# Performance work log

Hardware: AMD Instinct MI355X
Metric: run time of the kernel (lower is better)

The kernel has to match this reference:

```python
import jax, jax.numpy as jnp
import numpy as np

B = 4
T, Hh, Ww = 16, 32, 32
C = 256
HEADS = 8
WIN = 4
SHIFT = 2
MLP = 1024


def _rel_pos_index(w):
    coords = np.stack(np.meshgrid(np.arange(w), np.arange(w), np.arange(w), indexing='ij')).reshape(3, -1)
    rc = (coords[:, :, None] - coords[:, None, :]).transpose(1, 2, 0)
    rc[:, :, 0] += w - 1
    rc[:, :, 1] += w - 1
    rc[:, :, 2] += w - 1
    rc[:, :, 0] *= (2 * w - 1) * (2 * w - 1)
    rc[:, :, 1] *= 2 * w - 1
    return rc.sum(-1).astype(np.int32)  # (w^3, w^3)


def _attn_mask(t, h, w, win, shift):
    m = np.zeros((t, h, w))
    sl = (slice(0, -win), slice(-win, -shift), slice(-shift, None))
    cnt = 0
    for a in sl:
        for b in sl:
            for c in sl:
                m[a, b, c] = cnt
                cnt += 1
    m = m.reshape(t // win, win, h // win, win, w // win, win).transpose(0, 2, 4, 1, 3, 5).reshape(-1, win ** 3)
    am = m[:, None, :] - m[:, :, None]  # (nW, N, N)
    return np.where(am != 0, -100.0, 0.0).astype(np.float32)


def setup_inputs() -> dict:
    key = jax.random.key(0)
    ks = jax.random.split(key, 12)
    s_in = 1.0 / np.sqrt(C)
    s_mlp = 1.0 / np.sqrt(MLP)
    return {
        'x': jax.random.normal(ks[0], (B, T * Hh * Ww, C), jnp.float32),
        'norm1_g': jnp.ones((C,), jnp.float32),
        'norm1_b': jnp.zeros((C,), jnp.float32),
        'qkv_w': jax.random.normal(ks[1], (C, 3 * C), jnp.float32) * s_in,
        'qkv_b': jax.random.normal(ks[2], (3 * C,), jnp.float32) * 0.02,
        'proj_w': jax.random.normal(ks[3], (C, C), jnp.float32) * s_in,
        'proj_b': jax.random.normal(ks[4], (C,), jnp.float32) * 0.02,
        'rel_bias_table': jax.random.normal(ks[5], ((2 * WIN - 1) ** 3, HEADS), jnp.float32) * 0.02,
        'norm2_g': jnp.ones((C,), jnp.float32),
        'norm2_b': jnp.zeros((C,), jnp.float32),
        'mlp_w1': jax.random.normal(ks[6], (C, MLP), jnp.float32) * s_in,
        'mlp_b1': jax.random.normal(ks[7], (MLP,), jnp.float32) * 0.02,
        'mlp_w2': jax.random.normal(ks[8], (MLP, C), jnp.float32) * s_mlp,
        'mlp_b2': jax.random.normal(ks[9], (C,), jnp.float32) * 0.02,
        'rel_index': jnp.asarray(_rel_pos_index(WIN)),
        'attn_mask': jnp.asarray(_attn_mask(T, Hh, Ww, WIN, SHIFT)),
    }


def _ln(x, g, b, eps):
    mu = x.mean(-1, keepdims=True)
    var = ((x - mu) ** 2).mean(-1, keepdims=True)
    return (x - mu) * jax.lax.rsqrt(var + eps) * g + b


def reference(x, norm1_g, norm1_b, qkv_w, qkv_b, proj_w, proj_b, rel_bias_table,
              norm2_g, norm2_b, mlp_w1, mlp_b1, mlp_w2, mlp_b2, rel_index, attn_mask):
    w = WIN
    N = w ** 3
    hd = C // HEADS
    scale = hd ** -0.5

    h = _ln(x, norm1_g, norm1_b, 1e-5).reshape(B, T, Hh, Ww, C)
    h = jnp.roll(h, shift=(-SHIFT, -SHIFT, -SHIFT), axis=(1, 2, 3))
    # window partition -> (B*nW, N, C)
    h = h.reshape(B, T // w, w, Hh // w, w, Ww // w, w, C)
    h = h.transpose(0, 1, 3, 5, 2, 4, 6, 7).reshape(-1, N, C)

    qkv = (h @ qkv_w + qkv_b).reshape(-1, N, 3, HEADS, hd)
    qkv = qkv.transpose(2, 0, 3, 1, 4)  # (3, BW, heads, N, hd)
    q, k, v = qkv[0] * scale, qkv[1], qkv[2]
    attn = jnp.einsum('bhid,bhjd->bhij', q, k)

    bias = rel_bias_table[rel_index.reshape(-1)].reshape(N, N, HEADS).transpose(2, 0, 1)
    attn = attn + bias[None]

    nW = attn_mask.shape[0]
    attn = attn.reshape(-1, nW, HEADS, N, N) + attn_mask[None, :, None]
    attn = jax.nn.softmax(attn.reshape(-1, HEADS, N, N), axis=-1)

    o = jnp.einsum('bhij,bhjd->bhid', attn, v).transpose(0, 2, 1, 3).reshape(-1, N, C)
    o = o @ proj_w + proj_b
    # window reverse
    o = o.reshape(B, T // w, Hh // w, Ww // w, w, w, w, C)
    o = o.transpose(0, 1, 4, 2, 5, 3, 6, 7).reshape(B, T, Hh, Ww, C)
    o = jnp.roll(o, shift=(SHIFT, SHIFT, SHIFT), axis=(1, 2, 3)).reshape(B, T * Hh * Ww, C)

    x = x + o
    y = _ln(x, norm2_g, norm2_b, 1e-6)
    y = jax.nn.gelu(y @ mlp_w1 + mlp_b1, approximate=False) @ mlp_w2 + mlp_b2
    return x + y
```

## Files before the change

kernel.cpp:

```cpp
#include <hip/hip_runtime.h>
#include <cstdint>
#include <cstddef>

typedef float  f32x4_t  __attribute__((ext_vector_type(4)));
typedef __bf16 bf16x8_t __attribute__((ext_vector_type(8)));
typedef __bf16 bf16x4_t __attribute__((ext_vector_type(4)));

#define NTOK   65536
#define CCH    256
#define NWINT  1024

__device__ __forceinline__ float wred_sum(float v) {
#pragma unroll
  for (int off = 32; off > 0; off >>= 1) v += __shfl_xor(v, off, 64);
  return v;
}

__device__ __forceinline__ void gload16(void* lds, const void* g) {
  __builtin_amdgcn_global_load_lds(
      (const __attribute__((address_space(1))) uint32_t*)g,
      (__attribute__((address_space(3))) uint32_t*)lds, 16, 0, 0);
}

__device__ __forceinline__ int win_to_orig(int token) {
  int gid = token >> 6, n = token & 63;
  int bb = gid >> 8, rem = gid & 255;
  int t = (((rem >> 6) << 2) + (n >> 4) + 2) & 15;
  int h = ((((rem >> 3) & 7) << 2) + ((n >> 2) & 3) + 2) & 31;
  int w = (((rem & 7) << 2) + (n & 3) + 2) & 31;
  return ((bb * 16 + t) * 32 + h) * 32 + w;
}

__device__ __forceinline__ float gelu_f(float v) {
  float u = v * (0.7978845608028654f + 0.03567740814f * v * v);
  float t = 1.0f - 2.0f / (__expf(2.0f * u) + 1.0f);
  return 0.5f * v * (1.0f + t);
}

#define MFMA16(ACC, W, Af)                                              \
  _Pragma("unroll") for (int nn = 0; nn < 4; ++nn)                      \
      _Pragma("unroll") for (int mm = 0; mm < 4; ++mm)                  \
          ACC[nn][mm] = __builtin_amdgcn_mfma_f32_16x16x32_bf16(        \
              W[nn], Af[mm], ACC[nn][mm], 0, 0, 0);

__global__ __launch_bounds__(256) void prep_weights(
    const float* __restrict__ qkv_w, const float* __restrict__ proj_w,
    const float* __restrict__ mlp_w1, const float* __restrict__ mlp_w2,
    __bf16* __restrict__ wt_qkv, __bf16* __restrict__ wt_proj,
    __bf16* __restrict__ wt_mlp1, __bf16* __restrict__ wt_mlp2) {
  int i = blockIdx.x * 256 + threadIdx.x;
  if (i < 196608) {
    int k = i / 768, n = i % 768;
    wt_qkv[n * 256 + k] = (__bf16)qkv_w[i];
  } else if (i < 262144) {
    int j = i - 196608;
    int k = j >> 8, n = j & 255;
    wt_proj[n * 256 + k] = (__bf16)proj_w[j];
  } else if (i < 524288) {
    int j = i - 262144;
    int k = j >> 10, n = j & 1023;
    wt_mlp1[n * 256 + k] = (__bf16)mlp_w1[j];
  } else {
    int j = i - 524288;
    int k = j >> 8, n = j & 255;
    wt_mlp2[n * 1024 + k] = (__bf16)mlp_w2[j];
  }
}

__global__ __launch_bounds__(256) void cm_prep(
    const float* __restrict__ table, const int* __restrict__ ridx,
    const float* __restrict__ mask, __bf16* __restrict__ cm) {
  int tid = blockIdx.x * 256 + threadIdx.x;
  int l = tid & 63;
  int t16 = (tid >> 6) & 15;
  int h = (tid >> 10) & 7;
  int w = tid >> 13;
  int it = t16 & 3, jt = t16 >> 2;
  int i = it * 16 + (l & 15);
  int jb = jt * 16 + ((l >> 4) << 2);
  const float* mrow = mask + (size_t)w * 4096 + i * 64;
  const int* rrow = ridx + i * 64;
  bf16x4_t o;
#pragma unroll
  for (int r = 0; r < 4; ++r) {
    int j = jb + r;
    o[r] = (__bf16)(table[rrow[j] * 8 + h] + mrow[j]);
  }
  *(bf16x4_t*)(cm + (size_t)tid * 4) = o;
}

__global__ __launch_bounds__(256) void ln_kernel(
    const float* __restrict__ xin, const float* __restrict__ g,
    const float* __restrict__ b, __bf16* __restrict__ out, float eps) {
  int token = blockIdx.x * 4 + (threadIdx.x >> 6);
  int lane = threadIdx.x & 63;
  size_t src = (size_t)win_to_orig(token);
  f32x4_t v = ((const f32x4_t*)(xin + src * CCH))[lane];
  float mu = wred_sum(v[0] + v[1] + v[2] + v[3]) * (1.0f / 256.0f);
  float d0 = v[0] - mu, d1 = v[1] - mu, d2 = v[2] - mu, d3 = v[3] - mu;
  float var = wred_sum(d0 * d0 + d1 * d1 + d2 * d2 + d3 * d3) * (1.0f / 256.0f);
  float rs = rsqrtf(var + eps);
  f32x4_t gg = ((const f32x4_t*)g)[lane];
  f32x4_t bb = ((const f32x4_t*)b)[lane];
  bf16x4_t o;
  o[0] = (__bf16)(d0 * rs * gg[0] + bb[0]);
  o[1] = (__bf16)(d1 * rs * gg[1] + bb[1]);
  o[2] = (__bf16)(d2 * rs * gg[2] + bb[2]);
  o[3] = (__bf16)(d3 * rs * gg[3] + bb[3]);
  *(bf16x4_t*)(out + (size_t)token * CCH + lane * 4) = o;
}


__device__ __forceinline__ void stage_A64(__bf16* yA, const __bf16* A,
                                          int bm, int tid) {
#pragma unroll
  for (int rnd = 0; rnd < 8; ++rnd) {
    int slot = rnd * 256 + tid;
    int row = slot >> 5;
    int cb = ((slot & 31) << 4) ^ ((row & 7) << 4);
    gload16((char*)yA + slot * 16,
            (const char*)(A + (size_t)(bm + row) * 256) + cb);
  }
  asm volatile("s_waitcnt vmcnt(0)" ::: "memory");
  __syncthreads();
}

__global__ __launch_bounds__(256, 3) void gemm_qkv(
    const __bf16* __restrict__ A, const __bf16* __restrict__ Bt,
    const float* __restrict__ bias, __bf16* __restrict__ outp) {
  __shared__ __bf16 yA[64 * 256];
  const int wv = threadIdx.x >> 6;
  const int ln = threadIdx.x & 63;
  const int i15 = ln & 15, g = ln >> 4;
  const int sw = (i15 & 7) << 4;

  int nwg = gridDim.x;
  int wgid = ((int)blockIdx.x & 7) * (nwg >> 3) + ((int)blockIdx.x >> 3);
  int bx = wgid % 3, by = wgid / 3;
  const int bm = by * 64, bn = bx * 256;

  stage_A64(yA, A, bm, (int)threadIdx.x);

  const __bf16* wP[4];
#pragma unroll
  for (int q = 0; q < 4; ++q)
    wP[q] = Bt + (size_t)(bn + wv * 64 + q * 16 + i15) * 256 + g * 8;

  f32x4_t acc[4][4];
#pragma unroll
  for (int nn = 0; nn < 4; ++nn)
#pragma unroll
    for (int mm = 0; mm < 4; ++mm) acc[nn][mm] = (f32x4_t){0.f, 0.f, 0.f, 0.f};

#pragma unroll
  for (int kt = 0; kt < 4; ++kt)
#pragma unroll
    for (int kh = 0; kh < 2; ++kh) {
      bf16x8_t wf[4], af[4];
#pragma unroll
      for (int nn = 0; nn < 4; ++nn)
        wf[nn] = *(const bf16x8_t*)(wP[nn] + kt * 64 + kh * 32);
#pragma unroll
      for (int mm = 0; mm < 4; ++mm)
        af[mm] = *(const bf16x8_t*)((const char*)yA + (mm * 16 + i15) * 512 +
                                    ((kt * 128 + kh * 64 + g * 16) ^ sw));
      MFMA16(acc, wf, af);
    }

#pragma unroll
  for (int nn = 0; nn < 4; ++nn) {
    int colg = bn + wv * 64 + nn * 16 + g * 4;
    f32x4_t bv = *(const f32x4_t*)(bias + colg);
#pragma unroll
    for (int mm = 0; mm < 4; ++mm) {
      int rowg = bm + mm * 16 + i15;
      bf16x4_t o;
#pragma unroll
      for (int r = 0; r < 4; ++r) o[r] = (__bf16)(acc[nn][mm][r] + bv[r]);
      *(bf16x4_t*)(outp + (size_t)rowg * 768 + colg) = o;
    }
  }
}

__global__ __launch_bounds__(256, 3) void proj_ln(
    const __bf16* __restrict__ A, const __bf16* __restrict__ Bt,
    const float* __restrict__ bias, const float* __restrict__ res,
    const float* __restrict__ g2, const float* __restrict__ b2,
    __bf16* __restrict__ x2b, __bf16* __restrict__ yb) {
  __shared__ __bf16 yA[64 * 256];
  __shared__ float2 stf[256];
  const int wv = threadIdx.x >> 6;
  const int ln = threadIdx.x & 63;
  const int i15 = ln & 15, g = ln >> 4;
  const int sw = (i15 & 7) << 4;

  int nwg = gridDim.x;
  int wgid = ((int)blockIdx.x & 7) * (nwg >> 3) + ((int)blockIdx.x >> 3);
  const int bm = wgid * 64;

  stage_A64(yA, A, bm, (int)threadIdx.x);

  const __bf16* wP[4];
#pragma unroll
  for (int q = 0; q < 4; ++q)
    wP[q] = Bt + (size_t)(wv * 64 + q * 16 + i15) * 256 + g * 8;

  f32x4_t acc[4][4];
#pragma unroll
  for (int nn = 0; nn < 4; ++nn)
#pragma unroll
    for (int mm = 0; mm < 4; ++mm) acc[nn][mm] = (f32x4_t){0.f, 0.f, 0.f, 0.f};

#pragma unroll
  for (int kt = 0; kt < 4; ++kt)
#pragma unroll
    for (int kh = 0; kh < 2; ++kh) {
      bf16x8_t wf[4], af[4];
#pragma unroll
      for (int nn = 0; nn < 4; ++nn)
        wf[nn] = *(const bf16x8_t*)(wP[nn] + kt * 64 + kh * 32);
#pragma unroll
      for (int mm = 0; mm < 4; ++mm)
        af[mm] = *(const bf16x8_t*)((const char*)yA + (mm * 16 + i15) * 512 +
                                    ((kt * 128 + kh * 64 + g * 16) ^ sw));
      MFMA16(acc, wf, af);
    }

  size_t dst[4];
#pragma unroll
  for (int mm = 0; mm < 4; ++mm)
    dst[mm] = (size_t)win_to_orig(bm + mm * 16 + i15) * CCH;
#pragma unroll
  for (int nn = 0; nn < 4; ++nn) {
    int colg = wv * 64 + nn * 16 + g * 4;
    f32x4_t bv = *(const f32x4_t*)(bias + colg);
#pragma unroll
    for (int mm = 0; mm < 4; ++mm) {
      f32x4_t rv = *(const f32x4_t*)(res + dst[mm] + colg);
#pragma unroll
      for (int r = 0; r < 4; ++r) acc[nn][mm][r] += bv[r] + rv[r];
    }
  }

#pragma unroll
  for (int mm = 0; mm < 4; ++mm) {
    float s1 = 0.f, s2 = 0.f;
#pragma unroll
    for (int nn = 0; nn < 4; ++nn)
#pragma unroll
      for (int r = 0; r < 4; ++r) {
        float v = acc[nn][mm][r];
        s1 += v;
        s2 += v * v;
      }
    s1 += __shfl_xor(s1, 16, 64);
    s1 += __shfl_xor(s1, 32, 64);
    s2 += __shfl_xor(s2, 16, 64);
    s2 += __shfl_xor(s2, 32, 64);
    if (g == 0) stf[(mm * 16 + i15) * 4 + wv] = make_float2(s1, s2);
  }
  __syncthreads();
  float mu[4], rs[4];
#pragma unroll
  for (int mm = 0; mm < 4; ++mm) {
    int row = mm * 16 + i15;
    float S1 = 0.f, S2 = 0.f;
#pragma unroll
    for (int w = 0; w < 4; ++w) {
      float2 p = stf[row * 4 + w];
      S1 += p.x;
      S2 += p.y;
    }
    mu[mm] = S1 * (1.0f / 256.0f);
    rs[mm] = rsqrtf(S2 * (1.0f / 256.0f) - mu[mm] * mu[mm] + 1e-6f);
  }

#pragma unroll
  for (int nn = 0; nn < 4; ++nn) {
    int colg = wv * 64 + nn * 16 + g * 4;
    f32x4_t gv = *(const f32x4_t*)(g2 + colg);
    f32x4_t bv = *(const f32x4_t*)(b2 + colg);
#pragma unroll
    for (int mm = 0; mm < 4; ++mm) {
      f32x4_t v = acc[nn][mm];
      bf16x4_t xo, yo;
#pragma unroll
      for (int r = 0; r < 4; ++r) {
        xo[r] = (__bf16)v[r];
        yo[r] = (__bf16)((v[r] - mu[mm]) * rs[mm] * gv[r] + bv[r]);
      }
      *(bf16x4_t*)(x2b + dst[mm] + colg) = xo;
      *(bf16x4_t*)(yb + dst[mm] + colg) = yo;
    }
  }
}

__global__ __launch_bounds__(256, 2) void mlp_fused(
    const __bf16* __restrict__ yb, const __bf16* __restrict__ w1t,
    const float* __restrict__ b1, const __bf16* __restrict__ w2t,
    const float* __restrict__ b2, const __bf16* __restrict__ x2b,
    float* __restrict__ out) {
  __shared__ __bf16 yA[64 * 256];
  __shared__ __bf16 h1b[64 * 256];
  const int wv = threadIdx.x >> 6;
  const int ln = threadIdx.x & 63;
  const int i15 = ln & 15, g = ln >> 4;
  const int sw = (i15 & 7) << 4;

  int nwg = gridDim.x;
  int wgid = ((int)blockIdx.x & 7) * (nwg >> 3) + ((int)blockIdx.x >> 3);
  const int bm = wgid * 64;

  stage_A64(yA, yb, bm, (int)threadIdx.x);

  const __bf16* w1P[4];
  const __bf16* w2P[4];
  int rowoff[4];
#pragma unroll
  for (int q = 0; q < 4; ++q) {
    w1P[q] = w1t + (size_t)(wv * 64 + q * 16 + i15) * 256 + g * 8;
    w2P[q] = w2t + (size_t)(wv * 64 + q * 16 + i15) * 1024 + g * 8;
    rowoff[q] = (q * 16 + i15) * 512;
  }

  f32x4_t acc2[4][4];
#pragma unroll
  for (int nn = 0; nn < 4; ++nn)
#pragma unroll
    for (int mm = 0; mm < 4; ++mm) acc2[nn][mm] = (f32x4_t){0.f, 0.f, 0.f, 0.f};

#pragma unroll
  for (int nc = 0; nc < 4; ++nc) {
    f32x4_t acc1[4][4];
#pragma unroll
    for (int nn = 0; nn < 4; ++nn)
#pragma unroll
      for (int mm = 0; mm < 4; ++mm)
        acc1[nn][mm] = (f32x4_t){0.f, 0.f, 0.f, 0.f};

    const __bf16* w1c0 = w1P[0] + nc * 65536;
    const __bf16* w1c1 = w1P[1] + nc * 65536;
    const __bf16* w1c2 = w1P[2] + nc * 65536;
    const __bf16* w1c3 = w1P[3] + nc * 65536;
#pragma unroll
    for (int kt = 0; kt < 4; ++kt)
#pragma unroll
      for (int kh = 0; kh < 2; ++kh) {
        bf16x8_t wf[4], af[4];
        wf[0] = *(const bf16x8_t*)(w1c0 + kt * 64 + kh * 32);
        wf[1] = *(const bf16x8_t*)(w1c1 + kt * 64 + kh * 32);
        wf[2] = *(const bf16x8_t*)(w1c2 + kt * 64 + kh * 32);
        wf[3] = *(const bf16x8_t*)(w1c3 + kt * 64 + kh * 32);
#pragma unroll
        for (int mm = 0; mm < 4; ++mm)
          af[mm] = *(const bf16x8_t*)((const char*)yA + (mm * 16 + i15) * 512 +
                                      ((kt * 128 + kh * 64 + g * 16) ^ sw));
        MFMA16(acc1, wf, af);
      }

    const float* b1g = b1 + nc * 256 + wv * 64;
#pragma unroll
    for (int nn = 0; nn < 4; ++nn) {
      f32x4_t bb = *(const f32x4_t*)(b1g + nn * 16 + g * 4);
#pragma unroll
      for (int mm = 0; mm < 4; ++mm) {
        bf16x4_t p;
#pragma unroll
        for (int r = 0; r < 4; ++r)
          p[r] = (__bf16)gelu_f(acc1[nn][mm][r] + bb[r]);
        *(bf16x4_t*)((char*)h1b + rowoff[mm] +
                     ((wv * 128 + nn * 32 + g * 8) ^ sw)) = p;
      }
    }
    __syncthreads();

#pragma unroll
    for (int ks = 0; ks < 8; ++ks) {
      bf16x8_t wf[4], hf[4];
#pragma unroll
      for (int nn = 0; nn < 4; ++nn)
        wf[nn] = *(const bf16x8_t*)(w2P[nn] + nc * 256 + ks * 32);
#pragma unroll
      for (int q = 0; q < 4; ++q)
        hf[q] = *(const bf16x8_t*)((const char*)h1b + rowoff[q] +
                                   ((ks * 64 + g * 16) ^ sw));
      MFMA16(acc2, wf, hf);
    }
    __syncthreads();
  }

#pragma unroll
  for (int nn = 0; nn < 4; ++nn) {
    int colg = wv * 64 + nn * 16 + g * 4;
    f32x4_t bb = *(const f32x4_t*)(b2 + colg);
#pragma unroll
    for (int mm = 0; mm < 4; ++mm) {
      int rowg = bm + mm * 16 + i15;
      bf16x4_t xv = *(const bf16x4_t*)(x2b + (size_t)rowg * 256 + colg);
      f32x4_t o;
#pragma unroll
      for (int r = 0; r < 4; ++r) o[r] = (float)xv[r] + acc2[nn][mm][r] + bb[r];
      *(f32x4_t*)(out + (size_t)rowg * 256 + colg) = o;
    }
  }
}

__global__ __launch_bounds__(256) void attn_mfma(
    const __bf16* __restrict__ qkv, const __bf16* __restrict__ cm,
    __bf16* __restrict__ owin) {
  __shared__ __align__(16) __bf16 smP[4][64 * 72];
  __shared__ __align__(16) __bf16 smV[4][64 * 32];
  const int wv = threadIdx.x >> 6;
  const int ln = threadIdx.x & 63;
  const int task = blockIdx.x * 4 + wv;
  const int win = task >> 3;
  const int h = task & 7;
  const int i15 = ln & 15, g = ln >> 4;

  const __bf16* base = qkv + (size_t)win * 64 * 768 + h * 32;

  {
    __bf16* vdst = smV[wv];
#pragma unroll
    for (int c = 0; c < 4; ++c) {
      const __bf16* src =
          base + (size_t)(c * 16 + (ln >> 2)) * 768 + 512 + (ln & 3) * 8;
      gload16(vdst + c * 512, src);
    }
  }

  bf16x8_t kf[4], qf[4];
#pragma unroll
  for (int t = 0; t < 4; ++t) {
    kf[t] = *(const bf16x8_t*)(base + (size_t)(t * 16 + i15) * 768 + 256 + g * 8);
    qf[t] = *(const bf16x8_t*)(base + (size_t)(t * 16 + i15) * 768 + g * 8);
  }

  f32x4_t st[4][4];
#pragma unroll
  for (int jt = 0; jt < 4; ++jt)
#pragma unroll
    for (int it = 0; it < 4; ++it)
      st[jt][it] = __builtin_amdgcn_mfma_f32_16x16x32_bf16(
          kf[jt], qf[it], (f32x4_t){0.f, 0.f, 0.f, 0.f}, 0, 0, 0);

  const __bf16* cmp = cm + (((size_t)(win & 255) * 8 + h) * 16) * 256;
#pragma unroll
  for (int jt = 0; jt < 4; ++jt)
#pragma unroll
    for (int it = 0; it < 4; ++it) {
      bf16x4_t c4 = *(const bf16x4_t*)(cmp + ((jt * 4 + it) * 64 + ln) * 4);
#pragma unroll
      for (int r = 0; r < 4; ++r)
        st[jt][it][r] =
            fmaf(st[jt][it][r], 0.17677669529663687f, (float)c4[r]);
    }

#pragma unroll
  for (int it = 0; it < 4; ++it) {
    float mx = -1e30f;
#pragma unroll
    for (int jt = 0; jt < 4; ++jt)
#pragma unroll
      for (int r = 0; r < 4; ++r) mx = fmaxf(mx, st[jt][it][r]);
    mx = fmaxf(mx, __shfl_xor(mx, 16, 64));
    mx = fmaxf(mx, __shfl_xor(mx, 32, 64));
    float sum = 0.f;
#pragma unroll
    for (int jt = 0; jt < 4; ++jt)
#pragma unroll
      for (int r = 0; r < 4; ++r) {
        float p = __expf(st[jt][it][r] - mx);
        st[jt][it][r] = p;
        sum += p;
      }
    sum += __shfl_xor(sum, 16, 64);
    sum += __shfl_xor(sum, 32, 64);
    float inv = 1.0f / sum;
#pragma unroll
    for (int jt = 0; jt < 4; ++jt) {
      bf16x4_t p4;
#pragma unroll
      for (int r = 0; r < 4; ++r) p4[r] = (__bf16)(st[jt][it][r] * inv);
      *(bf16x4_t*)(smP[wv] + (it * 16 + i15) * 72 + jt * 16 + g * 4) = p4;
    }
  }
  __syncthreads();

  f32x4_t oacc[4][2];
#pragma unroll
  for (int it = 0; it < 4; ++it)
#pragma unroll
    for (int dt = 0; dt < 2; ++dt) oacc[it][dt] = (f32x4_t){0.f, 0.f, 0.f, 0.f};

  const __bf16* pl = smP[wv];
  const __bf16* vl = smV[wv];
#pragma unroll
  for (int kt = 0; kt < 2; ++kt) {
    bf16x8_t vf[2];
#pragma unroll
    for (int dt = 0; dt < 2; ++dt)
#pragma unroll
      for (int e = 0; e < 8; ++e)
        vf[dt][e] = vl[(kt * 32 + g * 8 + e) * 32 + dt * 16 + i15];
#pragma unroll
    for (int it = 0; it < 4; ++it) {
      bf16x8_t pa =
          *(const bf16x8_t*)(pl + (it * 16 + i15) * 72 + kt * 32 + g * 8);
#pragma unroll
      for (int dt = 0; dt < 2; ++dt)
        oacc[it][dt] = __builtin_amdgcn_mfma_f32_16x16x32_bf16(
            pa, vf[dt], oacc[it][dt], 0, 0, 0);
    }
  }

  __bf16* op = owin + (size_t)win * 64 * 256 + h * 32;
#pragma unroll
  for (int it = 0; it < 4; ++it)
#pragma unroll
    for (int r = 0; r < 4; ++r) {
      int i = it * 16 + g * 4 + r;
#pragma unroll
      for (int dt = 0; dt < 2; ++dt)
        op[(size_t)i * 256 + dt * 16 + i15] = (__bf16)oacc[it][dt][r];
    }
}

extern "C" void kernel_launch(void* const* d_in, const int* in_sizes, int n_in,
                              void* d_out, int out_size, void* d_ws,
                              size_t ws_size, hipStream_t stream) {
  (void)in_sizes; (void)n_in; (void)out_size; (void)ws_size;
  const float* x      = (const float*)d_in[0];
  const float* n1g    = (const float*)d_in[1];
  const float* n1b    = (const float*)d_in[2];
  const float* qkv_w  = (const float*)d_in[3];
  const float* qkv_b  = (const float*)d_in[4];
  const float* proj_w = (const float*)d_in[5];
  const float* proj_b = (const float*)d_in[6];
  const float* rbt    = (const float*)d_in[7];
  const float* n2g    = (const float*)d_in[8];
  const float* n2b    = (const float*)d_in[9];
  const float* mlp_w1 = (const float*)d_in[10];
  const float* mlp_b1 = (const float*)d_in[11];
  const float* mlp_w2 = (const float*)d_in[12];
  const float* mlp_b2 = (const float*)d_in[13];
  const int*   ridx   = (const int*)d_in[14];
  const float* amask  = (const float*)d_in[15];

  char* ws = (char*)d_ws;
  size_t off = 0;
  auto alloc = [&](size_t bytes) {
    void* p = ws + off;
    off += (bytes + 255) & ~(size_t)255;
    return p;
  };
  __bf16* wt_qkv  = (__bf16*)alloc(768 * 256 * 2);
  __bf16* wt_proj = (__bf16*)alloc(256 * 256 * 2);
  __bf16* wt_mlp1 = (__bf16*)alloc(1024 * 256 * 2);
  __bf16* wt_mlp2 = (__bf16*)alloc(1024 * 256 * 2);
  __bf16* hwin = (__bf16*)alloc((size_t)NTOK * 256 * 2);
  __bf16* qkv  = (__bf16*)alloc((size_t)NTOK * 768 * 2);
  __bf16* owin = (__bf16*)alloc((size_t)NTOK * 256 * 2);
  __bf16* cmb  = hwin;
  __bf16* yb   = hwin;
  __bf16* x2b  = qkv;
  float* outp  = (float*)d_out;

  prep_weights<<<3072, 256, 0, stream>>>(qkv_w, proj_w, mlp_w1, mlp_w2,
                                         wt_qkv, wt_proj, wt_mlp1, wt_mlp2);
  ln_kernel<<<NTOK / 4, 256, 0, stream>>>(x, n1g, n1b, hwin, 1e-5f);
  gemm_qkv<<<3 * (NTOK / 64), 256, 0, stream>>>(hwin, wt_qkv, qkv_b, qkv);
  cm_prep<<<8192, 256, 0, stream>>>(rbt, ridx, amask, cmb);
  attn_mfma<<<2048, 256, 0, stream>>>(qkv, cmb, owin);
  proj_ln<<<NTOK / 64, 256, 0, stream>>>(owin, wt_proj, proj_b, x, n2g, n2b,
                                         x2b, yb);
  mlp_fused<<<NTOK / 64, 256, 0, stream>>>(yb, wt_mlp1, mlp_b1, wt_mlp2,
                                           mlp_b2, x2b, d_out ? outp : outp);
}
```

Measured before the change: 349.5 us.

## Halve GEMM row tiles to 32 and loop QKV column blocks inside one workgroup

Shrinks the M tile of the QKV, projection+LN and fused MLP kernels from 64 to 32 rows, doubling the grid and raising launch-bound occupancy to 4 workgroups per CU. QKV now stages each 32-row A tile once and loops over all three 256-column output blocks inside the workgroup, instead of launching a separate workgroup per column block. The intent is more parallelism, lower register and LDS pressure and better latency hiding. The cost is that the weight matrices are re-read from global/L2 twice as often per output row, and each MFMA batch is smaller, so there is less reuse per weight load.

```diff
diff --git a/kernel.cpp b/kernel.cpp
--- a/kernel.cpp
+++ b/kernel.cpp
@@ -37,9 +37,9 @@
   return 0.5f * v * (1.0f + t);
 }
 
-#define MFMA16(ACC, W, Af)                                              \
+#define MFMA8(ACC, W, Af)                                               \
   _Pragma("unroll") for (int nn = 0; nn < 4; ++nn)                      \
-      _Pragma("unroll") for (int mm = 0; mm < 4; ++mm)                  \
+      _Pragma("unroll") for (int mm = 0; mm < 2; ++mm)                  \
           ACC[nn][mm] = __builtin_amdgcn_mfma_f32_16x16x32_bf16(        \
               W[nn], Af[mm], ACC[nn][mm], 0, 0, 0);
 
@@ -111,10 +111,10 @@
 }
 
 
-__device__ __forceinline__ void stage_A64(__bf16* yA, const __bf16* A,
+__device__ __forceinline__ void stage_A32(__bf16* yA, const __bf16* A,
                                           int bm, int tid) {
 #pragma unroll
-  for (int rnd = 0; rnd < 8; ++rnd) {
+  for (int rnd = 0; rnd < 4; ++rnd) {
     int slot = rnd * 256 + tid;
     int row = slot >> 5;
     int cb = ((slot & 31) << 4) ^ ((row & 7) << 4);
@@ -125,10 +125,10 @@
   __syncthreads();
 }
 
-__global__ __launch_bounds__(256, 3) void gemm_qkv(
+__global__ __launch_bounds__(256, 4) void gemm_qkv(
     const __bf16* __restrict__ A, const __bf16* __restrict__ Bt,
     const float* __restrict__ bias, __bf16* __restrict__ outp) {
-  __shared__ __bf16 yA[64 * 256];
+  __shared__ __bf16 yA[32 * 256];
   const int wv = threadIdx.x >> 6;
   const int ln = threadIdx.x & 63;
   const int i15 = ln & 15, g = ln >> 4;
@@ -136,59 +136,62 @@
 
   int nwg = gridDim.x;
   int wgid = ((int)blockIdx.x & 7) * (nwg >> 3) + ((int)blockIdx.x >> 3);
-  int bx = wgid % 3, by = wgid / 3;
-  const int bm = by * 64, bn = bx * 256;
-
-  stage_A64(yA, A, bm, (int)threadIdx.x);
-
-  const __bf16* wP[4];
-#pragma unroll
-  for (int q = 0; q < 4; ++q)
-    wP[q] = Bt + (size_t)(bn + wv * 64 + q * 16 + i15) * 256 + g * 8;
-
-  f32x4_t acc[4][4];
-#pragma unroll
-  for (int nn = 0; nn < 4; ++nn)
-#pragma unroll
-    for (int mm = 0; mm < 4; ++mm) acc[nn][mm] = (f32x4_t){0.f, 0.f, 0.f, 0.f};
-
-#pragma unroll
-  for (int kt = 0; kt < 4; ++kt)
-#pragma unroll
-    for (int kh = 0; kh < 2; ++kh) {
-      bf16x8_t wf[4], af[4];
-#pragma unroll
-      for (int nn = 0; nn < 4; ++nn)
-        wf[nn] = *(const bf16x8_t*)(wP[nn] + kt * 64 + kh * 32);
-#pragma unroll
-      for (int mm = 0; mm < 4; ++mm)
-        af[mm] = *(const bf16x8_t*)((const char*)yA + (mm * 16 + i15) * 512 +
-                                    ((kt * 128 + kh * 64 + g * 16) ^ sw));
-      MFMA16(acc, wf, af);
-    }
-
-#pragma unroll
-  for (int nn = 0; nn < 4; ++nn) {
-    int colg = bn + wv * 64 + nn * 16 + g * 4;
-    f32x4_t bv = *(const f32x4_t*)(bias + colg);
-#pragma unroll
-    for (int mm = 0; mm < 4; ++mm) {
-      int rowg = bm + mm * 16 + i15;
-      bf16x4_t o;
-#pragma unroll
-      for (int r = 0; r < 4; ++r) o[r] = (__bf16)(acc[nn][mm][r] + bv[r]);
-      *(bf16x4_t*)(outp + (size_t)rowg * 768 + colg) = o;
-    }
-  }
-}
-
-__global__ __launch_bounds__(256, 3) void proj_ln(
+  const int bm = wgid * 32;
+
+  stage_A32(yA, A, bm, (int)threadIdx.x);
+
+#pragma unroll
+  for (int bx = 0; bx < 3; ++bx) {
+    const int bn = bx * 256;
+    const __bf16* wP[4];
+#pragma unroll
+    for (int q = 0; q < 4; ++q)
+      wP[q] = Bt + (size_t)(bn + wv * 64 + q * 16 + i15) * 256 + g * 8;
+
+    f32x4_t acc[4][2];
+#pragma unroll
+    for (int nn = 0; nn < 4; ++nn)
+#pragma unroll
+      for (int mm = 0; mm < 2; ++mm) acc[nn][mm] = (f32x4_t){0.f, 0.f, 0.f, 0.f};
+
+#pragma unroll
+    for (int kt = 0; kt < 4; ++kt)
+#pragma unroll
+      for (int kh = 0; kh < 2; ++kh) {
+        bf16x8_t wf[4], af[2];
+#pragma unroll
+        for (int nn = 0; nn < 4; ++nn)
+          wf[nn] = *(const bf16x8_t*)(wP[nn] + kt * 64 + kh * 32);
+#pragma unroll
+        for (int mm = 0; mm < 2; ++mm)
+          af[mm] = *(const bf16x8_t*)((const char*)yA + (mm * 16 + i15) * 512 +
+                                      ((kt * 128 + kh * 64 + g * 16) ^ sw));
+        MFMA8(acc, wf, af);
+      }
+
+#pragma unroll
+    for (int nn = 0; nn < 4; ++nn) {
+      int colg = bn + wv * 64 + nn * 16 + g * 4;
+      f32x4_t bv = *(const f32x4_t*)(bias + colg);
+#pragma unroll
+      for (int mm = 0; mm < 2; ++mm) {
+        int rowg = bm + mm * 16 + i15;
+        bf16x4_t o;
+#pragma unroll
+        for (int r = 0; r < 4; ++r) o[r] = (__bf16)(acc[nn][mm][r] + bv[r]);
+        *(bf16x4_t*)(outp + (size_t)rowg * 768 + colg) = o;
+      }
+    }
+  }
+}
+
+__global__ __launch_bounds__(256, 4) void proj_ln(
     const __bf16* __restrict__ A, const __bf16* __restrict__ Bt,
     const float* __restrict__ bias, const float* __restrict__ res,
     const float* __restrict__ g2, const float* __restrict__ b2,
     __bf16* __restrict__ x2b, __bf16* __restrict__ yb) {
-  __shared__ __bf16 yA[64 * 256];
-  __shared__ float2 stf[256];
+  __shared__ __bf16 yA[32 * 256];
+  __shared__ float2 stf[128];
   const int wv = threadIdx.x >> 6;
   const int ln = threadIdx.x & 63;
   const int i15 = ln & 15, g = ln >> 4;
@@ -196,46 +199,46 @@
 
   int nwg = gridDim.x;
   int wgid = ((int)blockIdx.x & 7) * (nwg >> 3) + ((int)blockIdx.x >> 3);
-  const int bm = wgid * 64;
-
-  stage_A64(yA, A, bm, (int)threadIdx.x);
+  const int bm = wgid * 32;
+
+  stage_A32(yA, A, bm, (int)threadIdx.x);
 
   const __bf16* wP[4];
 #pragma unroll
   for (int q = 0; q < 4; ++q)
     wP[q] = Bt + (size_t)(wv * 64 + q * 16 + i15) * 256 + g * 8;
 
-  f32x4_t acc[4][4];
+  f32x4_t acc[4][2];
 #pragma unroll
   for (int nn = 0; nn < 4; ++nn)
 #pragma unroll
-    for (int mm = 0; mm < 4; ++mm) acc[nn][mm] = (f32x4_t){0.f, 0.f, 0.f, 0.f};
+    for (int mm = 0; mm < 2; ++mm) acc[nn][mm] = (f32x4_t){0.f, 0.f, 0.f, 0.f};
 
 #pragma unroll
   for (int kt = 0; kt < 4; ++kt)
 #pragma unroll
     for (int kh = 0; kh < 2; ++kh) {
-      bf16x8_t wf[4], af[4];
+      bf16x8_t wf[4], af[2];
 #pragma unroll
       for (int nn = 0; nn < 4; ++nn)
         wf[nn] = *(const bf16x8_t*)(wP[nn] + kt * 64 + kh * 32);
 #pragma unroll
-      for (int mm = 0; mm < 4; ++mm)
+      for (int mm = 0; mm < 2; ++mm)
         af[mm] = *(const bf16x8_t*)((const char*)yA + (mm * 16 + i15) * 512 +
                                     ((kt * 128 + kh * 64 + g * 16) ^ sw));
-      MFMA16(acc, wf, af);
-    }
-
-  size_t dst[4];
-#pragma unroll
-  for (int mm = 0; mm < 4; ++mm)
+      MFMA8(acc, wf, af);
+    }
+
+  size_t dst[2];
+#pragma unroll
+  for (int mm = 0; mm < 2; ++mm)
     dst[mm] = (size_t)win_to_orig(bm + mm * 16 + i15) * CCH;
 #pragma unroll
   for (int nn = 0; nn < 4; ++nn) {
     int colg = wv * 64 + nn * 16 + g * 4;
     f32x4_t bv = *(const f32x4_t*)(bias + colg);
 #pragma unroll
-    for (int mm = 0; mm < 4; ++mm) {
+    for (int mm = 0; mm < 2; ++mm) {
       f32x4_t rv = *(const f32x4_t*)(res + dst[mm] + colg);
 #pragma unroll
       for (int r = 0; r < 4; ++r) acc[nn][mm][r] += bv[r] + rv[r];
@@ -243,7 +246,7 @@
   }
 
 #pragma unroll
-  for (int mm = 0; mm < 4; ++mm) {
+  for (int mm = 0; mm < 2; ++mm) {
     float s1 = 0.f, s2 = 0.f;
 #pragma unroll
     for (int nn = 0; nn < 4; ++nn)
@@ -260,9 +263,9 @@
     if (g == 0) stf[(mm * 16 + i15) * 4 + wv] = make_float2(s1, s2);
   }
   __syncthreads();
-  float mu[4], rs[4];
-#pragma unroll
-  for (int mm = 0; mm < 4; ++mm) {
+  float mu[2], rs[2];
+#pragma unroll
+  for (int mm = 0; mm < 2; ++mm) {
     int row = mm * 16 + i15;
     float S1 = 0.f, S2 = 0.f;
 #pragma unroll
@@ -281,7 +284,7 @@
     f32x4_t gv = *(const f32x4_t*)(g2 + colg);
     f32x4_t bv = *(const f32x4_t*)(b2 + colg);
 #pragma unroll
-    for (int mm = 0; mm < 4; ++mm) {
+    for (int mm = 0; mm < 2; ++mm) {
       f32x4_t v = acc[nn][mm];
       bf16x4_t xo, yo;
 #pragma unroll
@@ -295,13 +298,13 @@
   }
 }
 
-__global__ __launch_bounds__(256, 2) void mlp_fused(
+__global__ __launch_bounds__(256, 4) void mlp_fused(
     const __bf16* __restrict__ yb, const __bf16* __restrict__ w1t,
     const float* __restrict__ b1, const __bf16* __restrict__ w2t,
     const float* __restrict__ b2, const __bf16* __restrict__ x2b,
     float* __restrict__ out) {
-  __shared__ __bf16 yA[64 * 256];
-  __shared__ __bf16 h1b[64 * 256];
+  __shared__ __bf16 yA[32 * 256];
+  __shared__ __bf16 h1b[32 * 256];
   const int wv = threadIdx.x >> 6;
   const int ln = threadIdx.x & 63;
   const int i15 = ln & 15, g = ln >> 4;
@@ -309,53 +312,49 @@
 
   int nwg = gridDim.x;
   int wgid = ((int)blockIdx.x & 7) * (nwg >> 3) + ((int)blockIdx.x >> 3);
-  const int bm = wgid * 64;
-
-  stage_A64(yA, yb, bm, (int)threadIdx.x);
+  const int bm = wgid * 32;
+
+  stage_A32(yA, yb, bm, (int)threadIdx.x);
 
   const __bf16* w1P[4];
   const __bf16* w2P[4];
-  int rowoff[4];
+  int rowoff[2];
 #pragma unroll
   for (int q = 0; q < 4; ++q) {
     w1P[q] = w1t + (size_t)(wv * 64 + q * 16 + i15) * 256 + g * 8;
     w2P[q] = w2t + (size_t)(wv * 64 + q * 16 + i15) * 1024 + g * 8;
-    rowoff[q] = (q * 16 + i15) * 512;
-  }
-
-  f32x4_t acc2[4][4];
+  }
+  rowoff[0] = i15 * 512;
+  rowoff[1] = (16 + i15) * 512;
+
+  f32x4_t acc2[4][2];
 #pragma unroll
   for (int nn = 0; nn < 4; ++nn)
 #pragma unroll
-    for (int mm = 0; mm < 4; ++mm) acc2[nn][mm] = (f32x4_t){0.f, 0.f, 0.f, 0.f};
+    for (int mm = 0; mm < 2; ++mm) acc2[nn][mm] = (f32x4_t){0.f, 0.f, 0.f, 0.f};
 
 #pragma unroll
   for (int nc = 0; nc < 4; ++nc) {
-    f32x4_t acc1[4][4];
+    f32x4_t acc1[4][2];
 #pragma unroll
     for (int nn = 0; nn < 4; ++nn)
 #pragma unroll
-      for (int mm = 0; mm < 4; ++mm)
+      for (int mm = 0; mm < 2; ++mm)
         acc1[nn][mm] = (f32x4_t){0.f, 0.f, 0.f, 0.f};
 
-    const __bf16* w1c0 = w1P[0] + nc * 65536;
-    const __bf16* w1c1 = w1P[1] + nc * 65536;
-    const __bf16* w1c2 = w1P[2] + nc * 65536;
-    const __bf16* w1c3 = w1P[3] + nc * 65536;
 #pragma unroll
     for (int kt = 0; kt < 4; ++kt)
 #pragma unroll
       for (int kh = 0; kh < 2; ++kh) {
-        bf16x8_t wf[4], af[4];
-        wf[0] = *(const bf16x8_t*)(w1c0 + kt * 64 + kh * 32);
-        wf[1] = *(const bf16x8_t*)(w1c1 + kt * 64 + kh * 32);
-        wf[2] = *(const bf16x8_t*)(w1c2 + kt * 64 + kh * 32);
-        wf[3] = *(const bf16x8_t*)(w1c3 + kt * 64 + kh * 32);
-#pragma unroll
-        for (int mm = 0; mm < 4; ++mm)
+        bf16x8_t wf[4], af[2];
+#pragma unroll
+        for (int nn = 0; nn < 4; ++nn)
+          wf[nn] = *(const bf16x8_t*)(w1P[nn] + nc * 65536 + kt * 64 + kh * 32);
+#pragma unroll
+        for (int mm = 0; mm < 2; ++mm)
           af[mm] = *(const bf16x8_t*)((const char*)yA + (mm * 16 + i15) * 512 +
                                       ((kt * 128 + kh * 64 + g * 16) ^ sw));
-        MFMA16(acc1, wf, af);
+        MFMA8(acc1, wf, af);
       }
 
     const float* b1g = b1 + nc * 256 + wv * 64;
@@ -363,7 +362,7 @@
     for (int nn = 0; nn < 4; ++nn) {
       f32x4_t bb = *(const f32x4_t*)(b1g + nn * 16 + g * 4);
 #pragma unroll
-      for (int mm = 0; mm < 4; ++mm) {
+      for (int mm = 0; mm < 2; ++mm) {
         bf16x4_t p;
 #pragma unroll
         for (int r = 0; r < 4; ++r)
@@ -376,15 +375,15 @@
 
 #pragma unroll
     for (int ks = 0; ks < 8; ++ks) {
-      bf16x8_t wf[4], hf[4];
+      bf16x8_t wf[4], hf[2];
 #pragma unroll
       for (int nn = 0; nn < 4; ++nn)
         wf[nn] = *(const bf16x8_t*)(w2P[nn] + nc * 256 + ks * 32);
 #pragma unroll
-      for (int q = 0; q < 4; ++q)
+      for (int q = 0; q < 2; ++q)
         hf[q] = *(const bf16x8_t*)((const char*)h1b + rowoff[q] +
                                    ((ks * 64 + g * 16) ^ sw));
-      MFMA16(acc2, wf, hf);
+      MFMA8(acc2, wf, hf);
     }
     __syncthreads();
   }
@@ -394,7 +393,7 @@
     int colg = wv * 64 + nn * 16 + g * 4;
     f32x4_t bb = *(const f32x4_t*)(b2 + colg);
 #pragma unroll
-    for (int mm = 0; mm < 4; ++mm) {
+    for (int mm = 0; mm < 2; ++mm) {
       int rowg = bm + mm * 16 + i15;
       bf16x4_t xv = *(const bf16x4_t*)(x2b + (size_t)rowg * 256 + colg);
       f32x4_t o;
@@ -569,11 +568,11 @@
   prep_weights<<<3072, 256, 0, stream>>>(qkv_w, proj_w, mlp_w1, mlp_w2,
                                          wt_qkv, wt_proj, wt_mlp1, wt_mlp2);
   ln_kernel<<<NTOK / 4, 256, 0, stream>>>(x, n1g, n1b, hwin, 1e-5f);
-  gemm_qkv<<<3 * (NTOK / 64), 256, 0, stream>>>(hwin, wt_qkv, qkv_b, qkv);
+  gemm_qkv<<<NTOK / 32, 256, 0, stream>>>(hwin, wt_qkv, qkv_b, qkv);
   cm_prep<<<8192, 256, 0, stream>>>(rbt, ridx, amask, cmb);
   attn_mfma<<<2048, 256, 0, stream>>>(qkv, cmb, owin);
-  proj_ln<<<NTOK / 64, 256, 0, stream>>>(owin, wt_proj, proj_b, x, n2g, n2b,
+  proj_ln<<<NTOK / 32, 256, 0, stream>>>(owin, wt_proj, proj_b, x, n2g, n2b,
                                          x2b, yb);
-  mlp_fused<<<NTOK / 64, 256, 0, stream>>>(yb, wt_mlp1, mlp_b1, wt_mlp2,
-                                           mlp_b2, x2b, d_out ? outp : outp);
-}
+  mlp_fused<<<NTOK / 32, 256, 0, stream>>>(yb, wt_mlp1, mlp_b1, wt_mlp2,
+                                           mlp_b2, x2b, outp);
+}
```

After: 495.7 us. +41.8%, slower.
